# Kernel optimization log

Hardware: AMD Instinct MI355X
Metric: run time of the kernel (lower is better)

Reference implementation:

```python
import jax, jax.numpy as jnp
import numpy as np

N = 50000      # num nodes
E = 800000     # num edges
F_IN = 128     # CONFIG.FeatureLen()
H = 100        # conv1_hide
C = 16         # CONFIG.ClassNum()
LEAKY = 0.01


def setup_inputs() -> dict:
    key = jax.random.key(0)
    k = jax.random.split(key, 4)
    x = jax.random.normal(k[0], (N, F_IN), dtype=jnp.float32)
    edge_index = jax.random.randint(k[1], (2, E), 0, N, dtype=jnp.int32)
    W1 = jax.random.normal(k[2], (F_IN, H), dtype=jnp.float32) / np.sqrt(F_IN).astype(np.float32)
    b1 = jnp.zeros((H,), dtype=jnp.float32)
    W2 = jax.random.normal(k[3], (H, C), dtype=jnp.float32) / np.sqrt(H).astype(np.float32)
    b2 = jnp.zeros((C,), dtype=jnp.float32)
    return {"x": x, "W1": W1, "b1": b1, "W2": W2, "b2": b2, "edge_index": edge_index}


def _gcn_conv(x, W, b, src, dst):
    """PyG GCNConv: x' = D^{-1/2}(A+I)D^{-1/2} X W + b (symmetric norm, self-loops)."""
    x = x @ W  # transform first (smaller feature dim for propagation)
    loop = jnp.arange(N, dtype=src.dtype)
    s = jnp.concatenate([src, loop])  # sources (message senders)
    d = jnp.concatenate([dst, loop])  # targets (message receivers)
    deg = jax.ops.segment_sum(jnp.ones_like(d, dtype=x.dtype), d, num_segments=N)
    dinv = jnp.where(deg > 0, jax.lax.rsqrt(deg), 0.0)
    norm = dinv[s] * dinv[d]                      # [E+N]
    msg = x[s] * norm[:, None]                    # gather + scale
    out = jax.ops.segment_sum(msg, d, num_segments=N)  # scatter-add
    return out + b


def reference(x, W1, b1, W2, b2, edge_index):
    src, dst = edge_index[0], edge_index[1]
    h = _gcn_conv(x, W1, b1, src, dst)
    h = jax.nn.leaky_relu(h, negative_slope=LEAKY)
    # dropout is identity in eval mode (training=False)
    h = _gcn_conv(h, W2, b2, src, dst)
    return jax.nn.log_softmax(h, axis=1)
```

## Files before the change

kernel.cpp:

```cpp
#include <hip/hip_runtime.h>

#define F_IN 128
#define HDIM 100
#define HPAD 128
#define CDIM 16
#define CAP  64
#define BT_STRIDE 136
#define CHUNK 4096
#define KMAX 200
#define RCAP 64

static constexpr float LEAKY = 0.01f;

using short8  = __attribute__((ext_vector_type(8))) short;
using float4v = __attribute__((ext_vector_type(4))) float;
using float2v = __attribute__((ext_vector_type(2))) float;

__device__ __forceinline__ unsigned short f2bf(float f) {
    unsigned u = __float_as_uint(f);
    u += 0x7fffu + ((u >> 16) & 1u);
    return (unsigned short)(u >> 16);
}


__global__ __launch_bounds__(256) void k_gemm1_p1(const float* __restrict__ x,
                                                  const float* __restrict__ W1,
                                                  unsigned char* __restrict__ y1f8,
                                                  const int* __restrict__ src,
                                                  const int* __restrict__ dst,
                                                  unsigned* __restrict__ bkt_edges,
                                                  int* __restrict__ cnt_arr,
                                                  int N, int E, int FB, int KBKT) {
    __shared__ union {
        unsigned short bt[F_IN * BT_STRIDE];
        struct { unsigned stage[CHUNK]; int cnt[KMAX]; } p1;
    } sm;
    int bx = blockIdx.x;
    int t = threadIdx.x;

    if (bx < FB) {
        unsigned* stage = sm.p1.stage;
        int* cnt = sm.p1.cnt;
        for (int i = t; i < KBKT; i += 256) cnt[i] = 0;
        __syncthreads();
        int e0 = bx * CHUNK, e1 = min(E, e0 + CHUNK);
        for (int i = e0 + t; i < e1; i += 256) {
            int d = dst[i];
            unsigned pk = ((unsigned)d << 16) | (unsigned)src[i];
            atomicAdd(&cnt[d >> 8], 1);
            stage[i - e0] = pk;
        }
        __syncthreads();
        for (int i = t; i < KBKT; i += 256) cnt_arr[bx * KBKT + i] = cnt[i];
        __syncthreads();
        for (int i = t; i < KBKT; i += 256) cnt[i] = 0;
        __syncthreads();
        int m = e1 - e0;
        for (int i = t; i < m; i += 256) {
            unsigned pk = stage[i];
            int b = pk >> 24;
            int pos = atomicAdd(&cnt[b], 1);
            if (pos < RCAP)
                bkt_edges[((size_t)b * FB + bx) * RCAP + pos] = pk;
        }
        return;
    }

    for (int idx = t; idx < F_IN * HPAD; idx += 256) {
        int k = idx >> 7;
        int n = idx & 127;
        float v = (n < HDIM) ? W1[k * HDIM + n] : 0.f;
        sm.bt[n * BT_STRIDE + k] = f2bf(v);
    }
    __syncthreads();

    int wave = t >> 6, lane = t & 63;
    int Mtiles = (N + 15) >> 4;
    int tile = (bx - FB) * 4 + wave;
    if (tile >= Mtiles) return;
    int row0 = tile * 16;

    int m = lane & 15;
    int kq = lane >> 4;
    int arow = min(row0 + m, N - 1);
    const float* xrow = x + (size_t)arow * F_IN;

    short8 afrag[4];
    #pragma unroll
    for (int kt = 0; kt < 4; ++kt) {
        int kb = kt * 32 + kq * 8;
        float4 a0 = *(const float4*)(xrow + kb);
        float4 a1 = *(const float4*)(xrow + kb + 4);
        short8 f;
        f[0] = (short)f2bf(a0.x); f[1] = (short)f2bf(a0.y);
        f[2] = (short)f2bf(a0.z); f[3] = (short)f2bf(a0.w);
        f[4] = (short)f2bf(a1.x); f[5] = (short)f2bf(a1.y);
        f[6] = (short)f2bf(a1.z); f[7] = (short)f2bf(a1.w);
        afrag[kt] = f;
    }

    bool full = (row0 + 15 < N);
    #pragma unroll
    for (int ct = 0; ct < 8; ++ct) {
        float4v acc = {0.f, 0.f, 0.f, 0.f};
        #pragma unroll
        for (int kt = 0; kt < 4; ++kt) {
            short8 b = *(const short8*)&sm.bt[(ct * 16 + m) * BT_STRIDE + kt * 32 + kq * 8];
            acc = __builtin_amdgcn_mfma_f32_16x16x32_bf16(afrag[kt], b, acc, 0, 0, 0);
        }
        #pragma unroll
        for (int i = 0; i < 4; ++i) {
            int r = row0 + kq * 4 + i;
            int v8 = __builtin_amdgcn_cvt_pk_fp8_f32(acc[i], acc[i], 0, false);
            if (full || r < N)
                y1f8[(size_t)r * HPAD + ct * 16 + m] = (unsigned char)(v8 & 0xff);
        }
    }
}


__global__ __launch_bounds__(256) void k_p2(const unsigned* __restrict__ bkt_edges,
                                            const int* __restrict__ cnt_arr,
                                            int* __restrict__ deg,
                                            unsigned short* __restrict__ slots,
                                            int N, int FB, int KBKT) {
    __shared__ int cur[256];
    int b = blockIdx.x, t = threadIdx.x;
    cur[t] = 0;
    __syncthreads();
    for (int fb = t; fb < FB; fb += 256) {
        int c = cnt_arr[fb * KBKT + b];
        size_t base = ((size_t)b * FB + fb) * RCAP;
        for (int j = 0; j < c; ++j) {
            unsigned pk = bkt_edges[base + j];
            int d = pk >> 16;
            int pos = atomicAdd(&cur[d & 255], 1);
            if (pos < CAP)
                slots[(size_t)d * CAP + pos] = (unsigned short)(pk & 0xffffu);
        }
    }
    __syncthreads();
    int n = (b << 8) + t;
    if (n < N) deg[n] = cur[t];
}


__global__ __launch_bounds__(256) void k_agg1y2(const unsigned* __restrict__ y1u,
                                                const float* __restrict__ b1,
                                                const float* __restrict__ W2,
                                                const int* __restrict__ deg,
                                                const unsigned short* __restrict__ slots,
                                                float* __restrict__ y2, int N) {
    __shared__ float W2s[HDIM * CDIM];
    __shared__ float hs[4][2][HPAD];
    int t = threadIdx.x;
    for (int idx = t; idx < HDIM * CDIM; idx += 256) W2s[idx] = W2[idx];
    __syncthreads();

    int wave = t >> 6, lane = t & 63;
    int half = lane >> 5, l = lane & 31;
    int hbase = lane & 32;
    int n = blockIdx.x * 8 + wave * 2 + half;
    bool valid = (n < N);
    int nn = valid ? n : (N - 1);

    int beg = nn * CAP;
    int cnt = valid ? deg[nn] : 0;
    float dn = rsqrtf((float)deg[nn] + 1.0f);

    int cother = __shfl(cnt, lane ^ 32);
    int cmax = max(cnt, cother);

    float a0 = 0.f, a1 = 0.f, a2 = 0.f, a3 = 0.f;
    for (int e0 = 0; e0 < cmax; e0 += 32) {
        int mm = min(32, cnt - e0);
        unsigned su = 0u; float wv = 0.f;
        if (l < mm) {
            su = slots[beg + e0 + l];
            wv = rsqrtf((float)deg[su] + 1.0f);
        }
        int mmax = min(32, cmax - e0);
        int mpad = (mmax + 7) & ~7;
        for (int j = 0; j < mpad; j += 8) {
            float w[8]; unsigned vv[8];
            #pragma unroll
            for (int q = 0; q < 8; ++q) {
                int ln = hbase | (j + q);
                unsigned s = (unsigned)__shfl((int)su, ln);
                w[q] = __shfl(wv, ln);
                vv[q] = y1u[(size_t)s * 32 + l];
            }
            #pragma unroll
            for (int q = 0; q < 8; ++q) {
                float2v lov = __builtin_amdgcn_cvt_pk_f32_fp8((int)vv[q], false);
                float2v hiv = __builtin_amdgcn_cvt_pk_f32_fp8((int)vv[q], true);
                a0 = fmaf(w[q], lov[0], a0);
                a1 = fmaf(w[q], lov[1], a1);
                a2 = fmaf(w[q], hiv[0], a2);
                a3 = fmaf(w[q], hiv[1], a3);
            }
        }
    }
    {
        unsigned vn = y1u[(size_t)nn * 32 + l];
        float2v lov = __builtin_amdgcn_cvt_pk_f32_fp8((int)vn, false);
        float2v hiv = __builtin_amdgcn_cvt_pk_f32_fp8((int)vn, true);
        a0 = fmaf(dn, lov[0], a0);
        a1 = fmaf(dn, lov[1], a1);
        a2 = fmaf(dn, hiv[0], a2);
        a3 = fmaf(dn, hiv[1], a3);
    }

    float4 bb = (l < 25) ? *(const float4*)&b1[4 * l] : make_float4(0.f, 0.f, 0.f, 0.f);
    float h0 = fmaf(dn, a0, bb.x);
    float h1 = fmaf(dn, a1, bb.y);
    float h2 = fmaf(dn, a2, bb.z);
    float h3 = fmaf(dn, a3, bb.w);
    h0 = h0 > 0.f ? h0 : LEAKY * h0;
    h1 = h1 > 0.f ? h1 : LEAKY * h1;
    h2 = h2 > 0.f ? h2 : LEAKY * h2;
    h3 = h3 > 0.f ? h3 : LEAKY * h3;
    *(float4*)&hs[wave][half][4 * l] = make_float4(h0, h1, h2, h3);
    __builtin_amdgcn_wave_barrier();

    int c = l & 15, kg = l >> 4;
    const float* hrow = hs[wave][half];
    float p = 0.f;
    #pragma unroll 10
    for (int j = 0; j < 50; ++j) {
        int k = 2 * j + kg;
        p = fmaf(hrow[k], W2s[k * CDIM + c], p);
    }
    p += __shfl_down(p, 16);
    if (l < 16 && valid) y2[(size_t)n * CDIM + c] = p;
}


__global__ __launch_bounds__(256) void k_agg2(const float* __restrict__ y2,
                                              const float* __restrict__ b2,
                                              const int* __restrict__ deg,
                                              const unsigned short* __restrict__ slots,
                                              float* __restrict__ out, int N) {
    int t = threadIdx.x;
    int wave = t >> 6, lane = t & 63;
    int sub = lane >> 4, c = lane & 15;
    int n = blockIdx.x * 16 + wave * 4 + sub;
    bool valid = (n < N);
    int nn = valid ? n : 0;

    int beg = nn * CAP;
    int cnt = valid ? deg[nn] : 0;
    float dn = rsqrtf((float)deg[nn] + 1.0f);
    float acc = dn * y2[(size_t)nn * CDIM + c];

    for (int e0 = 0; e0 < cnt; e0 += 16) {
        int mm = min(16, cnt - e0);
        unsigned su = 0u; float wv = 0.f;
        if (c < mm) {
            su = slots[beg + e0 + c];
            wv = rsqrtf((float)deg[su] + 1.0f);
        }
        int mpad = (mm + 3) & ~3;
        for (int j = 0; j < mpad; j += 4) {
            float w[4]; float v[4];
            #pragma unroll
            for (int q = 0; q < 4; ++q) {
                int ln = sub * 16 + j + q;
                unsigned s = (unsigned)__shfl((int)su, ln);
                w[q] = __shfl(wv, ln);
                v[q] = y2[(size_t)s * CDIM + c];
            }
            #pragma unroll
            for (int q = 0; q < 4; ++q) acc = fmaf(w[q], v[q], acc);
        }
    }

    float lg = fmaf(dn, acc, b2[c]);
    float mx = lg;
    #pragma unroll
    for (int k = 8; k; k >>= 1) mx = fmaxf(mx, __shfl_xor(mx, k));
    float ex = __expf(lg - mx);
    #pragma unroll
    for (int k = 8; k; k >>= 1) ex += __shfl_xor(ex, k);
    float lse = mx + __logf(ex);
    if (valid) out[(size_t)n * CDIM + c] = lg - lse;
}


extern "C" void kernel_launch(void* const* d_in, const int* in_sizes, int n_in,
                              void* d_out, int out_size, void* d_ws, size_t ws_size,
                              hipStream_t stream) {
    const float* x  = (const float*)d_in[0];
    const float* W1 = (const float*)d_in[1];
    const float* b1 = (const float*)d_in[2];
    const float* W2 = (const float*)d_in[3];
    const float* b2 = (const float*)d_in[4];
    const int*   ei = (const int*)d_in[5];

    const int N = in_sizes[0] / F_IN;
    const int E = in_sizes[5] / 2;
    const int* src = ei;
    const int* dst = ei + E;

    const int KBKT = (N + 255) >> 8;
    const int FB   = (E + CHUNK - 1) / CHUNK;

    char* ws = (char*)d_ws;
    size_t off = 0;
    auto alloc = [&](size_t bytes) {
        char* p = ws + off;
        off += (bytes + 255) & ~(size_t)255;
        return p;
    };
    int*            deg       = (int*)alloc((size_t)N * 4);
    unsigned char*  y1f8      = (unsigned char*)alloc((size_t)N * HPAD);
    float*          y2        = (float*)alloc((size_t)N * CDIM * 4);
    unsigned short* slots     = (unsigned short*)alloc((size_t)N * CAP * 2);
    int*            cnt_arr   = (int*)alloc((size_t)FB * KBKT * 4);
    unsigned*       bkt_edges = (unsigned*)alloc((size_t)KBKT * FB * RCAP * 4);
    (void)ws_size; (void)n_in; (void)out_size;

    int Mtiles = (N + 15) / 16;
    int GG = (Mtiles + 3) / 4;

    k_gemm1_p1<<<FB + GG, 256, 0, stream>>>(x, W1, y1f8, src, dst,
                                            bkt_edges, cnt_arr, N, E, FB, KBKT);
    k_p2<<<KBKT, 256, 0, stream>>>(bkt_edges, cnt_arr, deg, slots, N, FB, KBKT);
    k_agg1y2<<<(N + 7) / 8, 256, 0, stream>>>((const unsigned*)y1f8, b1, W2,
                                              deg, slots, y2, N);
    k_agg2<<<(N + 15) / 16, 256, 0, stream>>>(y2, b2, deg, slots,
                                              (float*)d_out, N);
}
```

Measured before the change: 161.3 us.

## Merge bucket scatter and both aggregations into one cooperative persistent kernel

Replaces the three kernels k_p2, k_agg1y2 and k_agg2 with a single cooperative kernel that uses grid.sync() between the bucket-to-slots pass, the layer-1 aggregation plus W2 projection, and the layer-2 aggregation with log-softmax. Blocks loop persistently over work instead of launching one block per node group. The GEMM part of the first kernel becomes a grid-stride loop over a fixed 262 blocks. The aim is to cut launch gaps and tail overhead between stages. In exchange it pays for grid-wide barriers, and occupancy is limited to what fits cooperatively, capped at 2048 blocks.

```diff
diff --git a/kernel.cpp b/kernel.cpp
--- a/kernel.cpp
+++ b/kernel.cpp
@@ -1,4 +1,7 @@
 #include <hip/hip_runtime.h>
+#include <hip/hip_cooperative_groups.h>
+
+namespace cg = cooperative_groups;
 
 #define F_IN 128
 #define HDIM 100
@@ -30,7 +33,7 @@
                                                   const int* __restrict__ dst,
                                                   unsigned* __restrict__ bkt_edges,
                                                   int* __restrict__ cnt_arr,
-                                                  int N, int E, int FB, int KBKT) {
+                                                  int N, int E, int FB, int KBKT, int GB) {
     __shared__ union {
         unsigned short bt[F_IN * BT_STRIDE];
         struct { unsigned stage[CHUNK]; int cnt[KMAX]; } p1;
@@ -76,214 +79,217 @@
 
     int wave = t >> 6, lane = t & 63;
     int Mtiles = (N + 15) >> 4;
-    int tile = (bx - FB) * 4 + wave;
-    if (tile >= Mtiles) return;
-    int row0 = tile * 16;
-
     int m = lane & 15;
     int kq = lane >> 4;
-    int arow = min(row0 + m, N - 1);
-    const float* xrow = x + (size_t)arow * F_IN;
-
-    short8 afrag[4];
-    #pragma unroll
-    for (int kt = 0; kt < 4; ++kt) {
-        int kb = kt * 32 + kq * 8;
-        float4 a0 = *(const float4*)(xrow + kb);
-        float4 a1 = *(const float4*)(xrow + kb + 4);
-        short8 f;
-        f[0] = (short)f2bf(a0.x); f[1] = (short)f2bf(a0.y);
-        f[2] = (short)f2bf(a0.z); f[3] = (short)f2bf(a0.w);
-        f[4] = (short)f2bf(a1.x); f[5] = (short)f2bf(a1.y);
-        f[6] = (short)f2bf(a1.z); f[7] = (short)f2bf(a1.w);
-        afrag[kt] = f;
-    }
-
-    bool full = (row0 + 15 < N);
-    #pragma unroll
-    for (int ct = 0; ct < 8; ++ct) {
-        float4v acc = {0.f, 0.f, 0.f, 0.f};
+
+    for (int tile = (bx - FB) * 4 + wave; tile < Mtiles; tile += 4 * GB) {
+        int row0 = tile * 16;
+        int arow = min(row0 + m, N - 1);
+        const float* xrow = x + (size_t)arow * F_IN;
+
+        short8 afrag[4];
         #pragma unroll
         for (int kt = 0; kt < 4; ++kt) {
-            short8 b = *(const short8*)&sm.bt[(ct * 16 + m) * BT_STRIDE + kt * 32 + kq * 8];
-            acc = __builtin_amdgcn_mfma_f32_16x16x32_bf16(afrag[kt], b, acc, 0, 0, 0);
-        }
+            int kb = kt * 32 + kq * 8;
+            float4 a0 = *(const float4*)(xrow + kb);
+            float4 a1 = *(const float4*)(xrow + kb + 4);
+            short8 f;
+            f[0] = (short)f2bf(a0.x); f[1] = (short)f2bf(a0.y);
+            f[2] = (short)f2bf(a0.z); f[3] = (short)f2bf(a0.w);
+            f[4] = (short)f2bf(a1.x); f[5] = (short)f2bf(a1.y);
+            f[6] = (short)f2bf(a1.z); f[7] = (short)f2bf(a1.w);
+            afrag[kt] = f;
+        }
+
+        bool full = (row0 + 15 < N);
         #pragma unroll
-        for (int i = 0; i < 4; ++i) {
-            int r = row0 + kq * 4 + i;
-            int v8 = __builtin_amdgcn_cvt_pk_fp8_f32(acc[i], acc[i], 0, false);
-            if (full || r < N)
-                y1f8[(size_t)r * HPAD + ct * 16 + m] = (unsigned char)(v8 & 0xff);
+        for (int ct = 0; ct < 8; ++ct) {
+            float4v acc = {0.f, 0.f, 0.f, 0.f};
+            #pragma unroll
+            for (int kt = 0; kt < 4; ++kt) {
+                short8 b = *(const short8*)&sm.bt[(ct * 16 + m) * BT_STRIDE + kt * 32 + kq * 8];
+                acc = __builtin_amdgcn_mfma_f32_16x16x32_bf16(afrag[kt], b, acc, 0, 0, 0);
+            }
+            #pragma unroll
+            for (int i = 0; i < 4; ++i) {
+                int r = row0 + kq * 4 + i;
+                int v8 = __builtin_amdgcn_cvt_pk_fp8_f32(acc[i], acc[i], 0, false);
+                if (full || r < N)
+                    y1f8[(size_t)r * HPAD + ct * 16 + m] = (unsigned char)(v8 & 0xff);
+            }
         }
     }
 }
 
 
-__global__ __launch_bounds__(256) void k_p2(const unsigned* __restrict__ bkt_edges,
-                                            const int* __restrict__ cnt_arr,
-                                            int* __restrict__ deg,
-                                            unsigned short* __restrict__ slots,
-                                            int N, int FB, int KBKT) {
+__global__ __launch_bounds__(256) void k_coop(const unsigned* __restrict__ bkt_edges,
+                                              const int* __restrict__ cnt_arr,
+                                              const unsigned* __restrict__ y1u,
+                                              const float* __restrict__ b1,
+                                              const float* __restrict__ W2,
+                                              const float* __restrict__ b2,
+                                              int* __restrict__ deg,
+                                              unsigned short* __restrict__ slots,
+                                              float* __restrict__ y2,
+                                              float* __restrict__ out,
+                                              int N, int FB, int KBKT) {
     __shared__ int cur[256];
-    int b = blockIdx.x, t = threadIdx.x;
-    cur[t] = 0;
-    __syncthreads();
-    for (int fb = t; fb < FB; fb += 256) {
-        int c = cnt_arr[fb * KBKT + b];
-        size_t base = ((size_t)b * FB + fb) * RCAP;
-        for (int j = 0; j < c; ++j) {
-            unsigned pk = bkt_edges[base + j];
-            int d = pk >> 16;
-            int pos = atomicAdd(&cur[d & 255], 1);
-            if (pos < CAP)
-                slots[(size_t)d * CAP + pos] = (unsigned short)(pk & 0xffffu);
-        }
-    }
-    __syncthreads();
-    int n = (b << 8) + t;
-    if (n < N) deg[n] = cur[t];
-}
-
-
-__global__ __launch_bounds__(256) void k_agg1y2(const unsigned* __restrict__ y1u,
-                                                const float* __restrict__ b1,
-                                                const float* __restrict__ W2,
-                                                const int* __restrict__ deg,
-                                                const unsigned short* __restrict__ slots,
-                                                float* __restrict__ y2, int N) {
     __shared__ float W2s[HDIM * CDIM];
     __shared__ float hs[4][2][HPAD];
+    cg::grid_group grid = cg::this_grid();
     int t = threadIdx.x;
+    int G = gridDim.x;
+
     for (int idx = t; idx < HDIM * CDIM; idx += 256) W2s[idx] = W2[idx];
-    __syncthreads();
+
+    if ((int)blockIdx.x < KBKT) {
+        int b = blockIdx.x;
+        cur[t] = 0;
+        __syncthreads();
+        for (int fb = t; fb < FB; fb += 256) {
+            int c = cnt_arr[fb * KBKT + b];
+            size_t base = ((size_t)b * FB + fb) * RCAP;
+            for (int j = 0; j < c; ++j) {
+                unsigned pk = bkt_edges[base + j];
+                int d = pk >> 16;
+                int pos = atomicAdd(&cur[d & 255], 1);
+                if (pos < CAP)
+                    slots[(size_t)d * CAP + pos] = (unsigned short)(pk & 0xffffu);
+            }
+        }
+        __syncthreads();
+        int n = (b << 8) + t;
+        if (n < N) deg[n] = cur[t];
+    }
+    __threadfence();
+    grid.sync();
 
     int wave = t >> 6, lane = t & 63;
     int half = lane >> 5, l = lane & 31;
     int hbase = lane & 32;
-    int n = blockIdx.x * 8 + wave * 2 + half;
-    bool valid = (n < N);
-    int nn = valid ? n : (N - 1);
-
-    int beg = nn * CAP;
-    int cnt = valid ? deg[nn] : 0;
-    float dn = rsqrtf((float)deg[nn] + 1.0f);
-
-    int cother = __shfl(cnt, lane ^ 32);
-    int cmax = max(cnt, cother);
-
-    float a0 = 0.f, a1 = 0.f, a2 = 0.f, a3 = 0.f;
-    for (int e0 = 0; e0 < cmax; e0 += 32) {
-        int mm = min(32, cnt - e0);
-        unsigned su = 0u; float wv = 0.f;
-        if (l < mm) {
-            su = slots[beg + e0 + l];
-            wv = rsqrtf((float)deg[su] + 1.0f);
-        }
-        int mmax = min(32, cmax - e0);
-        int mpad = (mmax + 7) & ~7;
-        for (int j = 0; j < mpad; j += 8) {
-            float w[8]; unsigned vv[8];
-            #pragma unroll
-            for (int q = 0; q < 8; ++q) {
-                int ln = hbase | (j + q);
-                unsigned s = (unsigned)__shfl((int)su, ln);
-                w[q] = __shfl(wv, ln);
-                vv[q] = y1u[(size_t)s * 32 + l];
-            }
-            #pragma unroll
-            for (int q = 0; q < 8; ++q) {
-                float2v lov = __builtin_amdgcn_cvt_pk_f32_fp8((int)vv[q], false);
-                float2v hiv = __builtin_amdgcn_cvt_pk_f32_fp8((int)vv[q], true);
-                a0 = fmaf(w[q], lov[0], a0);
-                a1 = fmaf(w[q], lov[1], a1);
-                a2 = fmaf(w[q], hiv[0], a2);
-                a3 = fmaf(w[q], hiv[1], a3);
-            }
-        }
-    }
-    {
-        unsigned vn = y1u[(size_t)nn * 32 + l];
-        float2v lov = __builtin_amdgcn_cvt_pk_f32_fp8((int)vn, false);
-        float2v hiv = __builtin_amdgcn_cvt_pk_f32_fp8((int)vn, true);
-        a0 = fmaf(dn, lov[0], a0);
-        a1 = fmaf(dn, lov[1], a1);
-        a2 = fmaf(dn, hiv[0], a2);
-        a3 = fmaf(dn, hiv[1], a3);
-    }
-
-    float4 bb = (l < 25) ? *(const float4*)&b1[4 * l] : make_float4(0.f, 0.f, 0.f, 0.f);
-    float h0 = fmaf(dn, a0, bb.x);
-    float h1 = fmaf(dn, a1, bb.y);
-    float h2 = fmaf(dn, a2, bb.z);
-    float h3 = fmaf(dn, a3, bb.w);
-    h0 = h0 > 0.f ? h0 : LEAKY * h0;
-    h1 = h1 > 0.f ? h1 : LEAKY * h1;
-    h2 = h2 > 0.f ? h2 : LEAKY * h2;
-    h3 = h3 > 0.f ? h3 : LEAKY * h3;
-    *(float4*)&hs[wave][half][4 * l] = make_float4(h0, h1, h2, h3);
-    __builtin_amdgcn_wave_barrier();
-
-    int c = l & 15, kg = l >> 4;
-    const float* hrow = hs[wave][half];
-    float p = 0.f;
-    #pragma unroll 10
-    for (int j = 0; j < 50; ++j) {
-        int k = 2 * j + kg;
-        p = fmaf(hrow[k], W2s[k * CDIM + c], p);
-    }
-    p += __shfl_down(p, 16);
-    if (l < 16 && valid) y2[(size_t)n * CDIM + c] = p;
-}
-
-
-__global__ __launch_bounds__(256) void k_agg2(const float* __restrict__ y2,
-                                              const float* __restrict__ b2,
-                                              const int* __restrict__ deg,
-                                              const unsigned short* __restrict__ slots,
-                                              float* __restrict__ out, int N) {
-    int t = threadIdx.x;
-    int wave = t >> 6, lane = t & 63;
+    int ngB = (N + 7) >> 3;
+    for (int g = blockIdx.x; g < ngB; g += G) {
+        int n = g * 8 + wave * 2 + half;
+        bool valid = (n < N);
+        int nn = valid ? n : (N - 1);
+
+        int beg = nn * CAP;
+        int cnt = valid ? deg[nn] : 0;
+        float dn = rsqrtf((float)deg[nn] + 1.0f);
+
+        int cother = __shfl(cnt, lane ^ 32);
+        int cmax = max(cnt, cother);
+
+        float a0 = 0.f, a1 = 0.f, a2 = 0.f, a3 = 0.f;
+        for (int e0 = 0; e0 < cmax; e0 += 32) {
+            int mm = min(32, cnt - e0);
+            unsigned su = 0u; float wv = 0.f;
+            if (l < mm) {
+                su = slots[beg + e0 + l];
+                wv = rsqrtf((float)deg[su] + 1.0f);
+            }
+            int mmax = min(32, cmax - e0);
+            int mpad = (mmax + 7) & ~7;
+            for (int j = 0; j < mpad; j += 8) {
+                float w[8]; unsigned vv[8];
+                #pragma unroll
+                for (int q = 0; q < 8; ++q) {
+                    int ln = hbase | (j + q);
+                    unsigned s = (unsigned)__shfl((int)su, ln);
+                    w[q] = __shfl(wv, ln);
+                    vv[q] = y1u[(size_t)s * 32 + l];
+                }
+                #pragma unroll
+                for (int q = 0; q < 8; ++q) {
+                    float2v lov = __builtin_amdgcn_cvt_pk_f32_fp8((int)vv[q], false);
+                    float2v hiv = __builtin_amdgcn_cvt_pk_f32_fp8((int)vv[q], true);
+                    a0 = fmaf(w[q], lov[0], a0);
+                    a1 = fmaf(w[q], lov[1], a1);
+                    a2 = fmaf(w[q], hiv[0], a2);
+                    a3 = fmaf(w[q], hiv[1], a3);
+                }
+            }
+        }
+        {
+            unsigned vn = y1u[(size_t)nn * 32 + l];
+            float2v lov = __builtin_amdgcn_cvt_pk_f32_fp8((int)vn, false);
+            float2v hiv = __builtin_amdgcn_cvt_pk_f32_fp8((int)vn, true);
+            a0 = fmaf(dn, lov[0], a0);
+            a1 = fmaf(dn, lov[1], a1);
+            a2 = fmaf(dn, hiv[0], a2);
+            a3 = fmaf(dn, hiv[1], a3);
+        }
+
+        float4 bb = (l < 25) ? *(const float4*)&b1[4 * l] : make_float4(0.f, 0.f, 0.f, 0.f);
+        float h0 = fmaf(dn, a0, bb.x);
+        float h1 = fmaf(dn, a1, bb.y);
+        float h2 = fmaf(dn, a2, bb.z);
+        float h3 = fmaf(dn, a3, bb.w);
+        h0 = h0 > 0.f ? h0 : LEAKY * h0;
+        h1 = h1 > 0.f ? h1 : LEAKY * h1;
+        h2 = h2 > 0.f ? h2 : LEAKY * h2;
+        h3 = h3 > 0.f ? h3 : LEAKY * h3;
+        *(float4*)&hs[wave][half][4 * l] = make_float4(h0, h1, h2, h3);
+        __builtin_amdgcn_wave_barrier();
+
+        int c = l & 15, kg = l >> 4;
+        const float* hrow = hs[wave][half];
+        float p = 0.f;
+        #pragma unroll 10
+        for (int j = 0; j < 50; ++j) {
+            int k = 2 * j + kg;
+            p = fmaf(hrow[k], W2s[k * CDIM + c], p);
+        }
+        p += __shfl_down(p, 16);
+        if (l < 16 && valid) y2[(size_t)n * CDIM + c] = p;
+    }
+    __threadfence();
+    grid.sync();
+
     int sub = lane >> 4, c = lane & 15;
-    int n = blockIdx.x * 16 + wave * 4 + sub;
-    bool valid = (n < N);
-    int nn = valid ? n : 0;
-
-    int beg = nn * CAP;
-    int cnt = valid ? deg[nn] : 0;
-    float dn = rsqrtf((float)deg[nn] + 1.0f);
-    float acc = dn * y2[(size_t)nn * CDIM + c];
-
-    for (int e0 = 0; e0 < cnt; e0 += 16) {
-        int mm = min(16, cnt - e0);
-        unsigned su = 0u; float wv = 0.f;
-        if (c < mm) {
-            su = slots[beg + e0 + c];
-            wv = rsqrtf((float)deg[su] + 1.0f);
-        }
-        int mpad = (mm + 3) & ~3;
-        for (int j = 0; j < mpad; j += 4) {
-            float w[4]; float v[4];
-            #pragma unroll
-            for (int q = 0; q < 4; ++q) {
-                int ln = sub * 16 + j + q;
-                unsigned s = (unsigned)__shfl((int)su, ln);
-                w[q] = __shfl(wv, ln);
-                v[q] = y2[(size_t)s * CDIM + c];
-            }
-            #pragma unroll
-            for (int q = 0; q < 4; ++q) acc = fmaf(w[q], v[q], acc);
-        }
-    }
-
-    float lg = fmaf(dn, acc, b2[c]);
-    float mx = lg;
-    #pragma unroll
-    for (int k = 8; k; k >>= 1) mx = fmaxf(mx, __shfl_xor(mx, k));
-    float ex = __expf(lg - mx);
-    #pragma unroll
-    for (int k = 8; k; k >>= 1) ex += __shfl_xor(ex, k);
-    float lse = mx + __logf(ex);
-    if (valid) out[(size_t)n * CDIM + c] = lg - lse;
+    int ngC = (N + 15) >> 4;
+    for (int g = blockIdx.x; g < ngC; g += G) {
+        int n = g * 16 + wave * 4 + sub;
+        bool valid = (n < N);
+        int nn = valid ? n : 0;
+
+        int beg = nn * CAP;
+        int cnt = valid ? deg[nn] : 0;
+        float dn = rsqrtf((float)deg[nn] + 1.0f);
+        float acc = dn * y2[(size_t)nn * CDIM + c];
+
+        for (int e0 = 0; e0 < cnt; e0 += 16) {
+            int mm = min(16, cnt - e0);
+            unsigned su = 0u; float wv = 0.f;
+            if (c < mm) {
+                su = slots[beg + e0 + c];
+                wv = rsqrtf((float)deg[su] + 1.0f);
+            }
+            int mpad = (mm + 3) & ~3;
+            for (int j = 0; j < mpad; j += 4) {
+                float w[4]; float v[4];
+                #pragma unroll
+                for (int q = 0; q < 4; ++q) {
+                    int ln = sub * 16 + j + q;
+                    unsigned s = (unsigned)__shfl((int)su, ln);
+                    w[q] = __shfl(wv, ln);
+                    v[q] = y2[(size_t)s * CDIM + c];
+                }
+                #pragma unroll
+                for (int q = 0; q < 4; ++q) acc = fmaf(w[q], v[q], acc);
+            }
+        }
+
+        float lg = fmaf(dn, acc, b2[c]);
+        float mx = lg;
+        #pragma unroll
+        for (int k = 8; k; k >>= 1) mx = fmaxf(mx, __shfl_xor(mx, k));
+        float ex = __expf(lg - mx);
+        #pragma unroll
+        for (int k = 8; k; k >>= 1) ex += __shfl_xor(ex, k);
+        float lse = mx + __logf(ex);
+        if (valid) out[(size_t)n * CDIM + c] = lg - lse;
+    }
 }
 
 
@@ -320,14 +326,29 @@
     unsigned*       bkt_edges = (unsigned*)alloc((size_t)KBKT * FB * RCAP * 4);
     (void)ws_size; (void)n_in; (void)out_size;
 
-    int Mtiles = (N + 15) / 16;
-    int GG = (Mtiles + 3) / 4;
-
-    k_gemm1_p1<<<FB + GG, 256, 0, stream>>>(x, W1, y1f8, src, dst,
-                                            bkt_edges, cnt_arr, N, E, FB, KBKT);
-    k_p2<<<KBKT, 256, 0, stream>>>(bkt_edges, cnt_arr, deg, slots, N, FB, KBKT);
-    k_agg1y2<<<(N + 7) / 8, 256, 0, stream>>>((const unsigned*)y1f8, b1, W2,
-                                              deg, slots, y2, N);
-    k_agg2<<<(N + 15) / 16, 256, 0, stream>>>(y2, b2, deg, slots,
-                                              (float*)d_out, N);
+    const int GB = 262;
+
+    static int coopBlocks = 0;
+    if (coopBlocks == 0) {
+        int nb = 0;
+        if (hipOccupancyMaxActiveBlocksPerMultiprocessor(
+                &nb, reinterpret_cast<const void*>(&k_coop), 256, 0) != hipSuccess || nb < 1)
+            nb = 2;
+        if (nb > 8) nb = 8;
+        coopBlocks = nb * 256;
+        if (coopBlocks > 2048) coopBlocks = 2048;
+    }
+
+    k_gemm1_p1<<<FB + GB, 256, 0, stream>>>(x, W1, y1f8, src, dst,
+                                            bkt_edges, cnt_arr, N, E, FB, KBKT, GB);
+
+    const unsigned* y1u = (const unsigned*)y1f8;
+    float* outp = (float*)d_out;
+    int Narg = N, FBarg = FB, KBarg = KBKT;
+    void* args[] = { (void*)&bkt_edges, (void*)&cnt_arr, (void*)&y1u,
+                     (void*)&b1, (void*)&W2, (void*)&b2,
+                     (void*)&deg, (void*)&slots, (void*)&y2, (void*)&outp,
+                     (void*)&Narg, (void*)&FBarg, (void*)&KBarg };
+    hipLaunchCooperativeKernel(reinterpret_cast<const void*>(&k_coop),
+                               dim3(coopBlocks), dim3(256), args, 0, stream);
 }
```

After: 605.1 us. 3.75x slower.
